# Optimization experiments

Measured on AMD Instinct MI355X. Metric: run time of the kernel, lower is better.

The kernel has to match this reference:

```python
import jax, jax.numpy as jnp
import numpy as np

N, D = 1024, 1024          # sensors, raw signal length
EMB, CC, TP, NH, L, FF = 128, 64, 16, 4, 2, 2048
HD = EMB // NH             # head dim = 32


def setup_inputs() -> dict:
    key = jax.random.key(0)
    ks = iter(jax.random.split(key, 64))
    rn = lambda shape, s=0.05: jax.random.normal(next(ks), shape, dtype=jnp.float32) * s
    return {
        "x": jax.random.normal(next(ks), (N, 1, D), dtype=jnp.float32),
        "conv1_w": rn((CC // 2, 1, 7), 0.3), "conv1_b": rn((CC // 2,)),
        "bn1_g": jnp.ones((CC // 2,)), "bn1_b": jnp.zeros((CC // 2,)),
        "bn1_m": jnp.zeros((CC // 2,)), "bn1_v": jnp.ones((CC // 2,)),
        "conv2_w": rn((CC, CC // 2, 5), 0.1), "conv2_b": rn((CC,)),
        "bn2_g": jnp.ones((CC,)), "bn2_b": jnp.zeros((CC,)),
        "bn2_m": jnp.zeros((CC,)), "bn2_v": jnp.ones((CC,)),
        "proj_w": rn((EMB, CC * TP)), "proj_b": rn((EMB,)),
        "attn_in_w": rn((L, 3 * EMB, EMB)), "attn_in_b": rn((L, 3 * EMB)),
        "attn_out_w": rn((L, EMB, EMB)), "attn_out_b": rn((L, EMB)),
        "ln1_g": jnp.ones((L, EMB)), "ln1_b": jnp.zeros((L, EMB)),
        "ff1_w": rn((L, FF, EMB)), "ff1_b": rn((L, FF)),
        "ff2_w": rn((L, EMB, FF)), "ff2_b": rn((L, EMB)),
        "ln2_g": jnp.ones((L, EMB)), "ln2_b": jnp.zeros((L, EMB)),
        "nh1_w": rn((EMB, EMB)), "nh1_b": rn((EMB,)),
        "nh2_w": rn((3, EMB)), "nh2_b": rn((3,)),
        "e1_w": rn((EMB, 2 * EMB)), "e1_b": rn((EMB,)),
        "e2_w": rn((1, EMB)), "e2_b": rn((1,)),
        "p1_w": rn((EMB, EMB)), "p1_b": rn((EMB,)),
        "p2_w": rn((EMB, EMB)), "p2_b": rn((EMB,)),
    }


def _conv1d(x, w, b, pad):
    y = jax.lax.conv_general_dilated(x, w, (1,), [(pad, pad)],
                                     dimension_numbers=("NCH", "OIH", "NCH"))
    return y + b[None, :, None]


def _bn(x, g, b, m, v):  # eval-mode BatchNorm1d, eps=1e-5
    return (x - m[None, :, None]) * (g / jnp.sqrt(v + 1e-5))[None, :, None] + b[None, :, None]


def _ln(x, g, b):  # LayerNorm over last dim, eps=1e-5
    mu = x.mean(-1, keepdims=True)
    var = ((x - mu) ** 2).mean(-1, keepdims=True)
    return (x - mu) / jnp.sqrt(var + 1e-5) * g + b


def reference(x, conv1_w, conv1_b, bn1_g, bn1_b, bn1_m, bn1_v,
              conv2_w, conv2_b, bn2_g, bn2_b, bn2_m, bn2_v,
              proj_w, proj_b, attn_in_w, attn_in_b, attn_out_w, attn_out_b,
              ln1_g, ln1_b, ff1_w, ff1_b, ff2_w, ff2_b, ln2_g, ln2_b,
              nh1_w, nh1_b, nh2_w, nh2_b, e1_w, e1_b, e2_w, e2_b,
              p1_w, p1_b, p2_w, p2_b):
    # ---- SensorTemporalEncoder: conv+BN+GELU x2, AdaptiveAvgPool1d(TP) ----
    h = jax.nn.gelu(_bn(_conv1d(x, conv1_w, conv1_b, 3), bn1_g, bn1_b, bn1_m, bn1_v), approximate=False)
    h = jax.nn.gelu(_bn(_conv1d(h, conv2_w, conv2_b, 2), bn2_g, bn2_b, bn2_m, bn2_v), approximate=False)
    h = h.reshape(N, CC, TP, D // TP).mean(-1)  # adaptive avg pool (D divisible by TP)
    z = h.reshape(N, CC * TP) @ proj_w.T + proj_b  # (N, EMB)

    # ---- TransformerEncoder (post-LN, relu FFN, eval: no dropout) ----
    t = z
    for l in range(L):
        qkv = t @ attn_in_w[l].T + attn_in_b[l]          # (N, 3*EMB)
        q, k, v = jnp.split(qkv, 3, axis=-1)
        q = q.reshape(N, NH, HD).transpose(1, 0, 2)      # (H, N, d)
        k = k.reshape(N, NH, HD).transpose(1, 0, 2)
        v = v.reshape(N, NH, HD).transpose(1, 0, 2)
        a = jax.nn.softmax(jnp.einsum("hnd,hmd->hnm", q, k) / (HD ** 0.5), axis=-1)
        o = jnp.einsum("hnm,hmd->hnd", a, v).transpose(1, 0, 2).reshape(N, EMB)
        t = _ln(t + o @ attn_out_w[l].T + attn_out_b[l], ln1_g[l], ln1_b[l])
        f = jax.nn.relu(t @ ff1_w[l].T + ff1_b[l]) @ ff2_w[l].T + ff2_b[l]
        t = _ln(t + f, ln2_g[l], ln2_b[l])

    # ---- node head ----
    node_logits = jax.nn.relu(t @ nh1_w.T + nh1_b) @ nh2_w.T + nh2_b  # (N, 3)

    # ---- all-pairs edge MLP: cat([hi,hj]) @ W1 == hi@W1[:,:E] + hj@W1[:,E:] ----
    hi = t @ e1_w[:, :EMB].T                 # (N, EMB)
    hj = t @ e1_w[:, EMB:].T                 # (N, EMB)
    pre = hi[:, None, :] + hj[None, :, :] + e1_b  # (N, N, EMB)
    edge_logits = (jax.nn.relu(pre) @ e2_w[0]) + e2_b[0]  # (N, N)

    # ---- projector on pre-transformer z ----
    proj = jax.nn.relu(z @ p1_w.T + p1_b) @ p2_w.T + p2_b  # (N, EMB)
    return (node_logits, edge_logits, proj)
```

## Files before the change

kernel.cpp:

```cpp
#include <hip/hip_runtime.h>
#include <math.h>


typedef float f32x4 __attribute__((ext_vector_type(4)));
typedef short bf16x8 __attribute__((ext_vector_type(8)));
typedef unsigned short u16;
typedef unsigned short us4 __attribute__((ext_vector_type(4)));
typedef unsigned int u32;

__device__ __forceinline__ float gelu_fast(float v) {
  float ax = fabsf(v) * 0.70710678118654752440f;
  float t = __builtin_amdgcn_rcpf(fmaf(0.3275911f, ax, 1.f));
  float p = fmaf(1.061405429f, t, -1.453152027f);
  p = fmaf(p, t, 1.421413741f);
  p = fmaf(p, t, -0.284496736f);
  p = fmaf(p, t, 0.254829592f);
  p = p * t;
  float e = __expf(-ax * ax);
  float erfa = fmaf(-p, e, 1.f);
  float erfv = copysignf(erfa, v);
  return 0.5f * v * (1.f + erfv);
}

__device__ __forceinline__ u16 to_bf16(float v) {
  u32 u = __float_as_uint(v);
  return (u16)((u + 0x7FFFu + ((u >> 16) & 1u)) >> 16);
}
__device__ __forceinline__ u32 packbf(float a, float b) {
  return (u32)to_bf16(a) | ((u32)to_bf16(b) << 16);
}

__global__ __launch_bounds__(256) void encoder_kernel(
    const float* __restrict__ x,
    const float* __restrict__ w1, const float* __restrict__ b1,
    const float* __restrict__ g1, const float* __restrict__ be1,
    const float* __restrict__ m1, const float* __restrict__ v1,
    const float* __restrict__ w2, const float* __restrict__ b2,
    const float* __restrict__ g2, const float* __restrict__ be2,
    const float* __restrict__ m2, const float* __restrict__ v2,
    u16* __restrict__ pooled_bf)
{
  const int blk = blockIdx.x;
  const int n = blk >> 1, hb = blk & 1;
  const int P0 = hb * 512;
  const int tid = threadIdx.x;

  __shared__ __align__(16) float xs[524];
  __shared__ __align__(16) u16 h1s[516 * 40];

  for (int s = tid; s < 522; s += 256) {
    int gp = P0 - 5 + s;
    xs[s] = (gp >= 0 && gp < 1024) ? x[n * 1024 + gp] : 0.f;
  }

  const int l = tid & 63;
  const int w = tid >> 6;
  const int col = l & 15;
  const int kh = l >> 4;
  const int oc = w * 16 + col;
  bf16x8 bf[5];
#pragma unroll
  for (int t = 0; t < 5; t++) {
#pragma unroll
    for (int e = 0; e < 8; e++)
      bf[t][e] = (short)to_bf16(w2[(oc * 32 + kh * 8 + e) * 5 + t]);
  }
  const float sc2 = g2[oc] * rsqrtf(v2[oc] + 1e-5f);
  const float sh2 = (b2[oc] - m2[oc]) * sc2 + be2[oc];

  const int ch = tid & 31;
  float wk[7];
#pragma unroll
  for (int k = 0; k < 7; k++) wk[k] = w1[ch * 7 + k];
  const float s1 = g1[ch] * rsqrtf(v1[ch] + 1e-5f);
  const float t1 = (b1[ch] - m1[ch]) * s1 + be1[ch];

  __syncthreads();

  const int rb = tid >> 5;
  for (int r = rb; r < 516; r += 8) {
    float acc = 0.f;
#pragma unroll
    for (int k = 0; k < 7; k++) acc += wk[k] * xs[r + k];
    int pos = P0 - 2 + r;
    u16 hv = to_bf16(gelu_fast(fmaf(acc, s1, t1)));
    h1s[r * 40 + ch] = (pos >= 0 && pos < 1024) ? hv : (u16)0;
  }
  __syncthreads();

  float pool = 0.f;
#pragma unroll 4
  for (int pt = 0; pt < 32; pt++) {
    f32x4 acc = {0.f, 0.f, 0.f, 0.f};
    const u16* ap = &h1s[(pt * 16 + col) * 40 + kh * 8];
#pragma unroll
    for (int t = 0; t < 5; t++) {
      bf16x8 af = *(const bf16x8*)(ap + t * 40);
      acc = __builtin_amdgcn_mfma_f32_16x16x32_bf16(af, bf[t], acc, 0, 0, 0);
    }
    float s = 0.f;
#pragma unroll
    for (int rr = 0; rr < 4; rr++) s += gelu_fast(fmaf(acc[rr], sc2, sh2));
    pool += s;
    if ((pt & 3) == 3) {
      pool += __shfl_xor(pool, 16);
      pool += __shfl_xor(pool, 32);
      if (l < 16)
        pooled_bf[(n * 64 + oc) * 16 + hb * 8 + (pt >> 2)] =
            to_bf16(pool * (1.f / 64.f));
      pool = 0.f;
    }
  }
}

__global__ __launch_bounds__(256) void wconv_kernel(
    const float* __restrict__ proj_w, const float* __restrict__ attn_in_w,
    const float* __restrict__ attn_out_w, const float* __restrict__ ff1_w,
    const float* __restrict__ ff2_w, const float* __restrict__ nh1_w,
    const float* __restrict__ e1_w, const float* __restrict__ e1_b,
    const float* __restrict__ p1_w, const float* __restrict__ p2_w,
    u16* __restrict__ wbf, float* __restrict__ wbias)
{
  if (blockIdx.x == 1360) {
    int j = threadIdx.x;
    wbias[j] = (j < 128) ? 0.f : e1_b[j - 128];
    return;
  }
  int i0 = (blockIdx.x * 256 + threadIdx.x) * 4;
  float v[4];
  if (i0 < 131072) {
    const float* s = proj_w + i0;
#pragma unroll
    for (int u = 0; u < 4; u++) v[u] = s[u];
  } else if (i0 < 229376) {
    const float* s = attn_in_w + (i0 - 131072);
#pragma unroll
    for (int u = 0; u < 4; u++) v[u] = s[u];
  } else if (i0 < 262144) {
    const float* s = attn_out_w + (i0 - 229376);
#pragma unroll
    for (int u = 0; u < 4; u++) v[u] = s[u];
  } else if (i0 < 786432) {
    const float* s = ff1_w + (i0 - 262144);
#pragma unroll
    for (int u = 0; u < 4; u++) v[u] = s[u];
  } else if (i0 < 1310720) {
    const float* s = ff2_w + (i0 - 786432);
#pragma unroll
    for (int u = 0; u < 4; u++) v[u] = s[u];
  } else if (i0 < 1327104) {
    const float* s = nh1_w + (i0 - 1310720);
#pragma unroll
    for (int u = 0; u < 4; u++) v[u] = s[u];
  } else if (i0 < 1359872) {
    int j = i0 - 1327104;
#pragma unroll
    for (int u = 0; u < 4; u++) {
      int idx = j + u, nn = idx >> 7, k = idx & 127;
      v[u] = e1_w[(nn & 127) * 256 + (nn >> 7) * 128 + k];
    }
  } else if (i0 < 1376256) {
    const float* s = p1_w + (i0 - 1359872);
#pragma unroll
    for (int u = 0; u < 4; u++) v[u] = s[u];
  } else {
    const float* s = p2_w + (i0 - 1376256);
#pragma unroll
    for (int u = 0; u < 4; u++) v[u] = s[u];
  }
  us4 o;
#pragma unroll
  for (int u = 0; u < 4; u++) o[u] = to_bf16(v[u]);
  *(us4*)(wbf + i0) = o;
}

template<int NR, bool RELU, bool VT>
__global__ __launch_bounds__(64) void mm_kernel(
    const u16* __restrict__ A, int lda,
    const u16* __restrict__ B, int ldb,
    const float* __restrict__ bias,
    float* __restrict__ Cf, u16* __restrict__ Cb, u16* __restrict__ vt,
    int ldc, int K)
{
  const int m0 = blockIdx.x * 32, n0 = blockIdx.y * (NR * 16);
  const int l = threadIdx.x;
  const int r = l & 15, kh = l >> 4;

  f32x4 acc[2][NR];
#pragma unroll
  for (int i = 0; i < 2; i++)
#pragma unroll
    for (int j = 0; j < NR; j++) acc[i][j] = (f32x4){0.f, 0.f, 0.f, 0.f};

  const u16* Ap0 = A + (size_t)(m0 + r) * lda + kh * 8;
  const u16* Ap1 = Ap0 + (size_t)16 * lda;
  const u16* Bp = B + (size_t)(n0 + r) * ldb + kh * 8;

  for (int k0 = 0; k0 < K; k0 += 32) {
    bf16x8 a0 = *(const bf16x8*)(Ap0 + k0);
    bf16x8 a1 = *(const bf16x8*)(Ap1 + k0);
    bf16x8 bfr[NR];
#pragma unroll
    for (int ni = 0; ni < NR; ni++)
      bfr[ni] = *(const bf16x8*)(Bp + (size_t)ni * 16 * ldb + k0);
#pragma unroll
    for (int ni = 0; ni < NR; ni++) {
      acc[0][ni] = __builtin_amdgcn_mfma_f32_16x16x32_bf16(a0, bfr[ni], acc[0][ni], 0, 0, 0);
      acc[1][ni] = __builtin_amdgcn_mfma_f32_16x16x32_bf16(a1, bfr[ni], acc[1][ni], 0, 0, 0);
    }
  }

#pragma unroll
  for (int mi = 0; mi < 2; mi++) {
#pragma unroll
    for (int ni = 0; ni < NR; ni++) {
#pragma unroll
      for (int reg = 0; reg < 4; reg++) {
        int row = m0 + mi * 16 + kh * 4 + reg;
        int colx = n0 + ni * 16 + r;
        float v = acc[mi][ni][reg];
        if (bias) v += bias[colx];
        if (RELU) v = fmaxf(v, 0.f);
        if (Cf) Cf[(size_t)row * ldc + colx] = v;
        if (Cb) Cb[(size_t)row * ldc + colx] = to_bf16(v);
        if (VT) {
          if (colx >= 256) {
            int hv = (colx - 256) >> 5, dv = (colx - 256) & 31;
            vt[(size_t)hv * 32768 + (size_t)dv * 1024 + row] = to_bf16(v);
          }
        }
      }
    }
  }
}

__global__ __launch_bounds__(64) void attn_kernel(
    const u16* __restrict__ qkv, const u16* __restrict__ vt,
    u16* __restrict__ attnO)
{
  const int h = blockIdx.y, q0 = blockIdx.x * 16;
  const int l = threadIdx.x, q = l & 15, g = l >> 4;
  const float iso = 0.17677669529663689f;

  bf16x8 qf = *(const bf16x8*)(qkv + (size_t)(q0 + q) * 384 + h * 32 + g * 8);
  const int kvo0 = 8 * (q >> 2) + (q & 3);
  const int kvo1 = kvo0 + 4;
  const u16* kbase = qkv + 128 + h * 32 + g * 8;
  const u16* vbase = vt + (size_t)h * 32768 + (size_t)q * 1024 + g * 8;

  f32x4 o0 = {0.f, 0.f, 0.f, 0.f}, o1 = {0.f, 0.f, 0.f, 0.f};
  float m = -1e30f, lsum = 0.f;
  const f32x4 zero = {0.f, 0.f, 0.f, 0.f};

  for (int kv0 = 0; kv0 < 1024; kv0 += 32) {
    bf16x8 k0f = *(const bf16x8*)(kbase + (size_t)(kv0 + kvo0) * 384);
    bf16x8 k1f = *(const bf16x8*)(kbase + (size_t)(kv0 + kvo1) * 384);
    f32x4 s0 = __builtin_amdgcn_mfma_f32_16x16x32_bf16(k0f, qf, zero, 0, 0, 0);
    f32x4 s1 = __builtin_amdgcn_mfma_f32_16x16x32_bf16(k1f, qf, zero, 0, 0, 0);

    float tm = fmaxf(fmaxf(fmaxf(s0[0], s0[1]), fmaxf(s0[2], s0[3])),
                     fmaxf(fmaxf(s1[0], s1[1]), fmaxf(s1[2], s1[3])));
    tm = fmaxf(tm, __shfl_xor(tm, 16));
    tm = fmaxf(tm, __shfl_xor(tm, 32));
    float mn = fmaxf(m, tm);
    float corr = __expf((m - mn) * iso);

    float e0[4], e1v[4], sum = 0.f;
#pragma unroll
    for (int j = 0; j < 4; j++) {
      e0[j] = __expf((s0[j] - mn) * iso);
      e1v[j] = __expf((s1[j] - mn) * iso);
      sum += e0[j] + e1v[j];
    }
    lsum = lsum * corr + sum;
#pragma unroll
    for (int j = 0; j < 4; j++) { o0[j] *= corr; o1[j] *= corr; }

    union { u32 u[4]; bf16x8 v; } P;
    P.u[0] = packbf(e0[0], e0[1]);
    P.u[1] = packbf(e0[2], e0[3]);
    P.u[2] = packbf(e1v[0], e1v[1]);
    P.u[3] = packbf(e1v[2], e1v[3]);

    bf16x8 v0 = *(const bf16x8*)(vbase + kv0);
    bf16x8 v1 = *(const bf16x8*)(vbase + 16 * 1024 + kv0);
    o0 = __builtin_amdgcn_mfma_f32_16x16x32_bf16(v0, P.v, o0, 0, 0, 0);
    o1 = __builtin_amdgcn_mfma_f32_16x16x32_bf16(v1, P.v, o1, 0, 0, 0);
    m = mn;
  }
  lsum += __shfl_xor(lsum, 16);
  lsum += __shfl_xor(lsum, 32);
  float inv = __builtin_amdgcn_rcpf(lsum);

  us4 w0, w1;
#pragma unroll
  for (int reg = 0; reg < 4; reg++) {
    w0[reg] = to_bf16(o0[reg] * inv);
    w1[reg] = to_bf16(o1[reg] * inv);
  }
  u16* outp = attnO + (size_t)(q0 + q) * 128 + h * 32 + 4 * g;
  *(us4*)outp = w0;
  *(us4*)(outp + 16) = w1;
}

template<int K>
__global__ __launch_bounds__(256) void owl_kernel(
    const u16* __restrict__ A, const u16* __restrict__ Bw,
    const float* __restrict__ bias, const float* __restrict__ Res,
    float* __restrict__ outF, u16* __restrict__ outB,
    const float* __restrict__ g_, const float* __restrict__ b_)
{
  __shared__ float ld[32][132];
  const int m0 = blockIdx.x * 32;
  const int tid = threadIdx.x;
  const int w = tid >> 6, l = tid & 63;
  const int r = l & 15, kg = l >> 4;

  f32x4 acc[2][2];
#pragma unroll
  for (int i = 0; i < 2; i++)
#pragma unroll
    for (int j = 0; j < 2; j++) acc[i][j] = (f32x4){0.f, 0.f, 0.f, 0.f};

  const u16* Ap0 = A + (size_t)(m0 + r) * K + kg * 8;
  const u16* Ap1 = Ap0 + (size_t)16 * K;
  const u16* Bp0 = Bw + (size_t)(w * 32 + r) * K + kg * 8;
  const u16* Bp1 = Bp0 + (size_t)16 * K;

#pragma unroll 4
  for (int k0 = 0; k0 < K; k0 += 32) {
    bf16x8 a0 = *(const bf16x8*)(Ap0 + k0);
    bf16x8 a1 = *(const bf16x8*)(Ap1 + k0);
    bf16x8 b0 = *(const bf16x8*)(Bp0 + k0);
    bf16x8 b1 = *(const bf16x8*)(Bp1 + k0);
    acc[0][0] = __builtin_amdgcn_mfma_f32_16x16x32_bf16(a0, b0, acc[0][0], 0, 0, 0);
    acc[0][1] = __builtin_amdgcn_mfma_f32_16x16x32_bf16(a0, b1, acc[0][1], 0, 0, 0);
    acc[1][0] = __builtin_amdgcn_mfma_f32_16x16x32_bf16(a1, b0, acc[1][0], 0, 0, 0);
    acc[1][1] = __builtin_amdgcn_mfma_f32_16x16x32_bf16(a1, b1, acc[1][1], 0, 0, 0);
  }

#pragma unroll
  for (int mi = 0; mi < 2; mi++)
#pragma unroll
    for (int ni = 0; ni < 2; ni++)
#pragma unroll
      for (int reg = 0; reg < 4; reg++) {
        int row = mi * 16 + kg * 4 + reg;
        int col = w * 32 + ni * 16 + r;
        ld[row][col] = acc[mi][ni][reg] + bias[col] +
                       Res[(size_t)(m0 + row) * 128 + col];
      }
  __syncthreads();

  const int row = tid >> 3, s8 = tid & 7;
  f32x4 vv[4];
  float sum = 0.f, ss = 0.f;
#pragma unroll
  for (int u = 0; u < 4; u++) {
    vv[u] = *(const f32x4*)&ld[row][s8 * 16 + u * 4];
#pragma unroll
    for (int j = 0; j < 4; j++) { sum += vv[u][j]; ss += vv[u][j] * vv[u][j]; }
  }
#pragma unroll
  for (int off = 1; off <= 4; off <<= 1) {
    sum += __shfl_xor(sum, off);
    ss += __shfl_xor(ss, off);
  }
  float mu = sum * (1.f / 128.f);
  float var = ss * (1.f / 128.f) - mu * mu;
  float inv = rsqrtf(var + 1e-5f);
  size_t base = (size_t)(m0 + row) * 128;
#pragma unroll
  for (int u = 0; u < 4; u++) {
    int c = s8 * 16 + u * 4;
    f32x4 gv = *(const f32x4*)(g_ + c);
    f32x4 bv = *(const f32x4*)(b_ + c);
    f32x4 o;
    us4 ob;
#pragma unroll
    for (int j = 0; j < 4; j++) {
      o[j] = (vv[u][j] - mu) * inv * gv[j] + bv[j];
      ob[j] = to_bf16(o[j]);
    }
    *(f32x4*)(outF + base + c) = o;
    *(us4*)(outB + base + c) = ob;
  }
}

__global__ __launch_bounds__(256) void nh2_kernel(
    const float* __restrict__ mid, const float* __restrict__ w,
    const float* __restrict__ b, float* __restrict__ out)
{
  int m = blockIdx.x * 256 + threadIdx.x;
  const float* row = mid + (size_t)m * 128;
  float a0 = 0.f, a1 = 0.f, a2 = 0.f;
#pragma unroll 4
  for (int k = 0; k < 128; k++) {
    float xv = row[k];
    a0 += xv * w[k]; a1 += xv * w[128 + k]; a2 += xv * w[256 + k];
  }
  out[m * 3 + 0] = a0 + b[0];
  out[m * 3 + 1] = a1 + b[1];
  out[m * 3 + 2] = a2 + b[2];
}

__global__ __launch_bounds__(256) void edge_kernel(
    const float* __restrict__ comb,
    const float* __restrict__ w, const float* __restrict__ e2b,
    float* __restrict__ out)
{
  const int i0 = blockIdx.x * 64;
  const int j0 = blockIdx.y * 32;
  __shared__ float his[128][64];
  __shared__ float hjs[128][32];
  const int tid = threadIdx.x;
  {
    int r = tid >> 2, c0 = (tid & 3) * 32;
#pragma unroll
    for (int u = 0; u < 8; u++) {
      float4 v = *(const float4*)(comb + (size_t)(i0 + r) * 256 + c0 + u * 4);
      his[c0 + u * 4 + 0][r] = v.x; his[c0 + u * 4 + 1][r] = v.y;
      his[c0 + u * 4 + 2][r] = v.z; his[c0 + u * 4 + 3][r] = v.w;
    }
  }
  {
    int r = tid >> 3, c0 = (tid & 7) * 16;
#pragma unroll
    for (int u = 0; u < 4; u++) {
      float4 v = *(const float4*)(comb + (size_t)(j0 + r) * 256 + 128 + c0 + u * 4);
      hjs[c0 + u * 4 + 0][r] = v.x; hjs[c0 + u * 4 + 1][r] = v.y;
      hjs[c0 + u * 4 + 2][r] = v.z; hjs[c0 + u * 4 + 3][r] = v.w;
    }
  }
  __syncthreads();
  const int il = (tid & 15) * 4, jl = (tid >> 4) * 2;
  float acc[4][2] = {{0.f,0.f},{0.f,0.f},{0.f,0.f},{0.f,0.f}};
  for (int e = 0; e < 128; e++) {
    float4 a = *(const float4*)&his[e][il];
    float2 bv = *(const float2*)&hjs[e][jl];
    float we = w[e];
    float av[4] = {a.x, a.y, a.z, a.w};
    float bb[2] = {bv.x, bv.y};
#pragma unroll
    for (int ii = 0; ii < 4; ii++)
#pragma unroll
      for (int jj = 0; jj < 2; jj++)
        acc[ii][jj] += fmaxf(av[ii] + bb[jj], 0.f) * we;
  }
  float eb = e2b[0];
#pragma unroll
  for (int ii = 0; ii < 4; ii++) {
    float2 vv = make_float2(acc[ii][0] + eb, acc[ii][1] + eb);
    *(float2*)(out + (size_t)(i0 + il + ii) * 1024 + j0 + jl) = vv;
  }
}

extern "C" void kernel_launch(void* const* d_in, const int* in_sizes, int n_in,
                              void* d_out, int out_size, void* d_ws, size_t ws_size,
                              hipStream_t stream)
{
  const float* x        = (const float*)d_in[0];
  const float* conv1_w  = (const float*)d_in[1];
  const float* conv1_b  = (const float*)d_in[2];
  const float* bn1_g    = (const float*)d_in[3];
  const float* bn1_b    = (const float*)d_in[4];
  const float* bn1_m    = (const float*)d_in[5];
  const float* bn1_v    = (const float*)d_in[6];
  const float* conv2_w  = (const float*)d_in[7];
  const float* conv2_b  = (const float*)d_in[8];
  const float* bn2_g    = (const float*)d_in[9];
  const float* bn2_b    = (const float*)d_in[10];
  const float* bn2_m    = (const float*)d_in[11];
  const float* bn2_v    = (const float*)d_in[12];
  const float* proj_w   = (const float*)d_in[13];
  const float* proj_b   = (const float*)d_in[14];
  const float* attn_in_w  = (const float*)d_in[15];
  const float* attn_in_b  = (const float*)d_in[16];
  const float* attn_out_w = (const float*)d_in[17];
  const float* attn_out_b = (const float*)d_in[18];
  const float* ln1_g    = (const float*)d_in[19];
  const float* ln1_b    = (const float*)d_in[20];
  const float* ff1_w    = (const float*)d_in[21];
  const float* ff1_b    = (const float*)d_in[22];
  const float* ff2_w    = (const float*)d_in[23];
  const float* ff2_b    = (const float*)d_in[24];
  const float* ln2_g    = (const float*)d_in[25];
  const float* ln2_b    = (const float*)d_in[26];
  const float* nh1_w    = (const float*)d_in[27];
  const float* nh1_b    = (const float*)d_in[28];
  const float* nh2_w    = (const float*)d_in[29];
  const float* nh2_b    = (const float*)d_in[30];
  const float* e1_w     = (const float*)d_in[31];
  const float* e1_b     = (const float*)d_in[32];
  const float* e2_w     = (const float*)d_in[33];
  const float* e2_b     = (const float*)d_in[34];
  const float* p1_w     = (const float*)d_in[35];
  const float* p1_b     = (const float*)d_in[36];
  const float* p2_w     = (const float*)d_in[37];
  const float* p2_b     = (const float*)d_in[38];

  float* ws = (float*)d_ws;

  u16*  wbf    = (u16*)ws;
  float* wbias = ws + 696320;
  float* z     = ws + 696576;
  u16*  z_bf   = (u16*)(ws + 827648);
  float* tS    = ws + 893184;
  u16*  t_bf   = (u16*)(ws + 1024256);
  u16*  qkv_bf = (u16*)(ws + 1089792);
  float* R     = ws + 1286400;
  u16*  pooled_bf = (u16*)R;
  u16*  attnO  = (u16*)R;
  u16*  vt     = (u16*)R + 131072;
  u16*  fb     = (u16*)R;
  float* nhmid = R;
  float* e1out = R + 131072;
  u16*  pmid   = (u16*)(R + 393216);

  float* out_node = (float*)d_out;
  float* out_edge = out_node + 3072;
  float* out_proj = out_edge + 1048576;

  float* nullf = nullptr; u16* nullb = nullptr;

  wconv_kernel<<<1361, 256, 0, stream>>>(
      proj_w, attn_in_w, attn_out_w, ff1_w, ff2_w, nh1_w, e1_w, e1_b,
      p1_w, p2_w, wbf, wbias);

  encoder_kernel<<<2048, 256, 0, stream>>>(
      x, conv1_w, conv1_b, bn1_g, bn1_b, bn1_m, bn1_v,
      conv2_w, conv2_b, bn2_g, bn2_b, bn2_m, bn2_v, pooled_bf);

  mm_kernel<2, false, false><<<dim3(32, 4), 64, 0, stream>>>(
      pooled_bf, 1024, wbf, 1024, proj_b, z, z_bf, nullb, 128, 1024);

  for (int l = 0; l < 2; l++) {
    const float* resIn = l ? tS : z;
    const u16* tin_bf = l ? t_bf : z_bf;
    mm_kernel<4, false, true><<<dim3(32, 6), 64, 0, stream>>>(
        tin_bf, 128, wbf + 131072 + l * 49152, 128, attn_in_b + l * 384,
        nullf, qkv_bf, vt, 384, 128);
    attn_kernel<<<dim3(64, 4), 64, 0, stream>>>(qkv_bf, vt, attnO);
    owl_kernel<128><<<32, 256, 0, stream>>>(
        attnO, wbf + 229376 + l * 16384, attn_out_b + l * 128, resIn,
        tS, t_bf, ln1_g + l * 128, ln1_b + l * 128);
    mm_kernel<4, true, false><<<dim3(32, 32), 64, 0, stream>>>(
        t_bf, 128, wbf + 262144 + l * 262144, 128, ff1_b + l * 2048,
        nullf, fb, nullb, 2048, 128);
    owl_kernel<2048><<<32, 256, 0, stream>>>(
        fb, wbf + 786432 + l * 262144, ff2_b + l * 128, tS,
        tS, t_bf, ln2_g + l * 128, ln2_b + l * 128);
  }

  mm_kernel<2, true, false><<<dim3(32, 4), 64, 0, stream>>>(
      t_bf, 128, wbf + 1310720, 128, nh1_b, nhmid, nullb, nullb, 128, 128);
  nh2_kernel<<<4, 256, 0, stream>>>(nhmid, nh2_w, nh2_b, out_node);

  mm_kernel<2, false, false><<<dim3(32, 8), 64, 0, stream>>>(
      t_bf, 128, wbf + 1327104, 128, wbias, e1out, nullb, nullb, 256, 128);
  edge_kernel<<<dim3(16, 32), 256, 0, stream>>>(e1out, e2_w, e2_b, out_edge);

  mm_kernel<2, true, false><<<dim3(32, 4), 64, 0, stream>>>(
      z_bf, 128, wbf + 1359872, 128, p1_b, nullf, pmid, nullb, 128, 128);
  mm_kernel<2, false, false><<<dim3(32, 4), 64, 0, stream>>>(
      pmid, 128, wbf + 1376256, 128, p2_b, out_proj, nullb, nullb, 128, 128);
}
```

Baseline: 447.6 us.

## Split FF2+LayerNorm into wider GEMM plus row-norm, prefetch attention K/V, compile-time K

The fused FF2 GEMM with LayerNorm ran on only 32 blocks. It is replaced by an mm_kernel launch over 64 blocks that writes pre-activations, followed by a separate warp-per-row residual LayerNorm kernel. The attention loop now double-buffers its K and V fragments by loading the next tile before computing on the current one. mm_kernel takes K as a template parameter with unroll 4, and nh2 spreads each row across four lanes with the weights staged in shared memory. The trade is an extra launch and an extra round trip of the FF2 output through global memory, in exchange for more parallelism and better load latency hiding.

```diff
diff --git a/kernel.cpp b/kernel.cpp
--- a/kernel.cpp
+++ b/kernel.cpp
@@ -174,13 +174,13 @@
   *(us4*)(wbf + i0) = o;
 }
 
-template<int NR, bool RELU, bool VT>
+template<int NR, int K, bool RELU, bool VT>
 __global__ __launch_bounds__(64) void mm_kernel(
     const u16* __restrict__ A, int lda,
     const u16* __restrict__ B, int ldb,
     const float* __restrict__ bias,
     float* __restrict__ Cf, u16* __restrict__ Cb, u16* __restrict__ vt,
-    int ldc, int K)
+    int ldc)
 {
   const int m0 = blockIdx.x * 32, n0 = blockIdx.y * (NR * 16);
   const int l = threadIdx.x;
@@ -196,6 +196,7 @@
   const u16* Ap1 = Ap0 + (size_t)16 * lda;
   const u16* Bp = B + (size_t)(n0 + r) * ldb + kh * 8;
 
+#pragma unroll 4
   for (int k0 = 0; k0 < K; k0 += 32) {
     bf16x8 a0 = *(const bf16x8*)(Ap0 + k0);
     bf16x8 a1 = *(const bf16x8*)(Ap1 + k0);
@@ -252,11 +253,20 @@
   float m = -1e30f, lsum = 0.f;
   const f32x4 zero = {0.f, 0.f, 0.f, 0.f};
 
+  bf16x8 k0c = *(const bf16x8*)(kbase + (size_t)kvo0 * 384);
+  bf16x8 k1c = *(const bf16x8*)(kbase + (size_t)kvo1 * 384);
+  bf16x8 v0c = *(const bf16x8*)(vbase);
+  bf16x8 v1c = *(const bf16x8*)(vbase + 16 * 1024);
+
   for (int kv0 = 0; kv0 < 1024; kv0 += 32) {
-    bf16x8 k0f = *(const bf16x8*)(kbase + (size_t)(kv0 + kvo0) * 384);
-    bf16x8 k1f = *(const bf16x8*)(kbase + (size_t)(kv0 + kvo1) * 384);
-    f32x4 s0 = __builtin_amdgcn_mfma_f32_16x16x32_bf16(k0f, qf, zero, 0, 0, 0);
-    f32x4 s1 = __builtin_amdgcn_mfma_f32_16x16x32_bf16(k1f, qf, zero, 0, 0, 0);
+    const int nx = (kv0 + 32 < 1024) ? kv0 + 32 : kv0;
+    bf16x8 k0n = *(const bf16x8*)(kbase + (size_t)(nx + kvo0) * 384);
+    bf16x8 k1n = *(const bf16x8*)(kbase + (size_t)(nx + kvo1) * 384);
+    bf16x8 v0n = *(const bf16x8*)(vbase + nx);
+    bf16x8 v1n = *(const bf16x8*)(vbase + 16 * 1024 + nx);
+
+    f32x4 s0 = __builtin_amdgcn_mfma_f32_16x16x32_bf16(k0c, qf, zero, 0, 0, 0);
+    f32x4 s1 = __builtin_amdgcn_mfma_f32_16x16x32_bf16(k1c, qf, zero, 0, 0, 0);
 
     float tm = fmaxf(fmaxf(fmaxf(s0[0], s0[1]), fmaxf(s0[2], s0[3])),
                      fmaxf(fmaxf(s1[0], s1[1]), fmaxf(s1[2], s1[3])));
@@ -282,11 +292,10 @@
     P.u[2] = packbf(e1v[0], e1v[1]);
     P.u[3] = packbf(e1v[2], e1v[3]);
 
-    bf16x8 v0 = *(const bf16x8*)(vbase + kv0);
-    bf16x8 v1 = *(const bf16x8*)(vbase + 16 * 1024 + kv0);
-    o0 = __builtin_amdgcn_mfma_f32_16x16x32_bf16(v0, P.v, o0, 0, 0, 0);
-    o1 = __builtin_amdgcn_mfma_f32_16x16x32_bf16(v1, P.v, o1, 0, 0, 0);
+    o0 = __builtin_amdgcn_mfma_f32_16x16x32_bf16(v0c, P.v, o0, 0, 0, 0);
+    o1 = __builtin_amdgcn_mfma_f32_16x16x32_bf16(v1c, P.v, o1, 0, 0, 0);
     m = mn;
+    k0c = k0n; k1c = k1n; v0c = v0n; v1c = v1n;
   }
   lsum += __shfl_xor(lsum, 16);
   lsum += __shfl_xor(lsum, 32);
@@ -303,7 +312,6 @@
   *(us4*)(outp + 16) = w1;
 }
 
-template<int K>
 __global__ __launch_bounds__(256) void owl_kernel(
     const u16* __restrict__ A, const u16* __restrict__ Bw,
     const float* __restrict__ bias, const float* __restrict__ Res,
@@ -322,13 +330,13 @@
 #pragma unroll
     for (int j = 0; j < 2; j++) acc[i][j] = (f32x4){0.f, 0.f, 0.f, 0.f};
 
-  const u16* Ap0 = A + (size_t)(m0 + r) * K + kg * 8;
-  const u16* Ap1 = Ap0 + (size_t)16 * K;
-  const u16* Bp0 = Bw + (size_t)(w * 32 + r) * K + kg * 8;
-  const u16* Bp1 = Bp0 + (size_t)16 * K;
-
-#pragma unroll 4
-  for (int k0 = 0; k0 < K; k0 += 32) {
+  const u16* Ap0 = A + (size_t)(m0 + r) * 128 + kg * 8;
+  const u16* Ap1 = Ap0 + (size_t)16 * 128;
+  const u16* Bp0 = Bw + (size_t)(w * 32 + r) * 128 + kg * 8;
+  const u16* Bp1 = Bp0 + (size_t)16 * 128;
+
+#pragma unroll
+  for (int k0 = 0; k0 < 128; k0 += 32) {
     bf16x8 a0 = *(const bf16x8*)(Ap0 + k0);
     bf16x8 a1 = *(const bf16x8*)(Ap1 + k0);
     bf16x8 b0 = *(const bf16x8*)(Bp0 + k0);
@@ -387,21 +395,63 @@
   }
 }
 
+__global__ __launch_bounds__(256) void ln2r_kernel(
+    const float* __restrict__ pre, float* __restrict__ tS, u16* __restrict__ t_bf,
+    const float* __restrict__ g_, const float* __restrict__ b_)
+{
+  int row = blockIdx.x * 4 + (threadIdx.x >> 6);
+  int lane = threadIdx.x & 63;
+  size_t idx = (size_t)row * 128 + lane * 2;
+  float2 pv = *(const float2*)(pre + idx);
+  float2 rv = *(const float2*)(tS + idx);
+  float vx = pv.x + rv.x, vy = pv.y + rv.y;
+  float s = vx + vy;
+#pragma unroll
+  for (int off = 32; off >= 1; off >>= 1) s += __shfl_xor(s, off);
+  float mu = s * (1.f / 128.f);
+  float dx = vx - mu, dy = vy - mu;
+  float q = dx * dx + dy * dy;
+#pragma unroll
+  for (int off = 32; off >= 1; off >>= 1) q += __shfl_xor(q, off);
+  float inv = rsqrtf(q * (1.f / 128.f) + 1e-5f);
+  float2 gv = *(const float2*)(g_ + lane * 2);
+  float2 bv = *(const float2*)(b_ + lane * 2);
+  float ox = dx * inv * gv.x + bv.x, oy = dy * inv * gv.y + bv.y;
+  tS[idx] = ox; tS[idx + 1] = oy;
+  t_bf[idx] = to_bf16(ox); t_bf[idx + 1] = to_bf16(oy);
+}
+
 __global__ __launch_bounds__(256) void nh2_kernel(
     const float* __restrict__ mid, const float* __restrict__ w,
     const float* __restrict__ b, float* __restrict__ out)
 {
-  int m = blockIdx.x * 256 + threadIdx.x;
-  const float* row = mid + (size_t)m * 128;
+  __shared__ float wsm[384];
+  for (int i = threadIdx.x; i < 384; i += 256) wsm[i] = w[i];
+  __syncthreads();
+  int r = blockIdx.x * 64 + (threadIdx.x >> 2);
+  int q = threadIdx.x & 3;
+  const float* rp = mid + (size_t)r * 128 + q * 32;
   float a0 = 0.f, a1 = 0.f, a2 = 0.f;
-#pragma unroll 4
-  for (int k = 0; k < 128; k++) {
-    float xv = row[k];
-    a0 += xv * w[k]; a1 += xv * w[128 + k]; a2 += xv * w[256 + k];
-  }
-  out[m * 3 + 0] = a0 + b[0];
-  out[m * 3 + 1] = a1 + b[1];
-  out[m * 3 + 2] = a2 + b[2];
+#pragma unroll
+  for (int u = 0; u < 8; u++) {
+    float4 v = *(const float4*)(rp + u * 4);
+    int k = q * 32 + u * 4;
+    float xv[4] = {v.x, v.y, v.z, v.w};
+#pragma unroll
+    for (int j = 0; j < 4; j++) {
+      a0 += xv[j] * wsm[k + j];
+      a1 += xv[j] * wsm[128 + k + j];
+      a2 += xv[j] * wsm[256 + k + j];
+    }
+  }
+  a0 += __shfl_xor(a0, 1); a0 += __shfl_xor(a0, 2);
+  a1 += __shfl_xor(a1, 1); a1 += __shfl_xor(a1, 2);
+  a2 += __shfl_xor(a2, 1); a2 += __shfl_xor(a2, 2);
+  if (q == 0) {
+    out[r * 3 + 0] = a0 + b[0];
+    out[r * 3 + 1] = a1 + b[1];
+    out[r * 3 + 2] = a2 + b[2];
+  }
 }
 
 __global__ __launch_bounds__(256) void edge_kernel(
@@ -508,7 +558,8 @@
   float* tS    = ws + 893184;
   u16*  t_bf   = (u16*)(ws + 1024256);
   u16*  qkv_bf = (u16*)(ws + 1089792);
-  float* R     = ws + 1286400;
+  float* pre   = ws + 1286400;
+  float* R     = ws + 1417472;
   u16*  pooled_bf = (u16*)R;
   u16*  attnO  = (u16*)R;
   u16*  vt     = (u16*)R + 131072;
@@ -531,37 +582,39 @@
       x, conv1_w, conv1_b, bn1_g, bn1_b, bn1_m, bn1_v,
       conv2_w, conv2_b, bn2_g, bn2_b, bn2_m, bn2_v, pooled_bf);
 
-  mm_kernel<2, false, false><<<dim3(32, 4), 64, 0, stream>>>(
-      pooled_bf, 1024, wbf, 1024, proj_b, z, z_bf, nullb, 128, 1024);
+  mm_kernel<2, 1024, false, false><<<dim3(32, 4), 64, 0, stream>>>(
+      pooled_bf, 1024, wbf, 1024, proj_b, z, z_bf, nullb, 128);
 
   for (int l = 0; l < 2; l++) {
     const float* resIn = l ? tS : z;
     const u16* tin_bf = l ? t_bf : z_bf;
-    mm_kernel<4, false, true><<<dim3(32, 6), 64, 0, stream>>>(
+    mm_kernel<4, 128, false, true><<<dim3(32, 6), 64, 0, stream>>>(
         tin_bf, 128, wbf + 131072 + l * 49152, 128, attn_in_b + l * 384,
-        nullf, qkv_bf, vt, 384, 128);
+        nullf, qkv_bf, vt, 384);
     attn_kernel<<<dim3(64, 4), 64, 0, stream>>>(qkv_bf, vt, attnO);
-    owl_kernel<128><<<32, 256, 0, stream>>>(
+    owl_kernel<<<32, 256, 0, stream>>>(
         attnO, wbf + 229376 + l * 16384, attn_out_b + l * 128, resIn,
         tS, t_bf, ln1_g + l * 128, ln1_b + l * 128);
-    mm_kernel<4, true, false><<<dim3(32, 32), 64, 0, stream>>>(
+    mm_kernel<4, 128, true, false><<<dim3(32, 32), 64, 0, stream>>>(
         t_bf, 128, wbf + 262144 + l * 262144, 128, ff1_b + l * 2048,
-        nullf, fb, nullb, 2048, 128);
-    owl_kernel<2048><<<32, 256, 0, stream>>>(
-        fb, wbf + 786432 + l * 262144, ff2_b + l * 128, tS,
-        tS, t_bf, ln2_g + l * 128, ln2_b + l * 128);
-  }
-
-  mm_kernel<2, true, false><<<dim3(32, 4), 64, 0, stream>>>(
-      t_bf, 128, wbf + 1310720, 128, nh1_b, nhmid, nullb, nullb, 128, 128);
-  nh2_kernel<<<4, 256, 0, stream>>>(nhmid, nh2_w, nh2_b, out_node);
-
-  mm_kernel<2, false, false><<<dim3(32, 8), 64, 0, stream>>>(
-      t_bf, 128, wbf + 1327104, 128, wbias, e1out, nullb, nullb, 256, 128);
+        nullf, fb, nullb, 2048);
+    mm_kernel<4, 2048, false, false><<<dim3(32, 2), 64, 0, stream>>>(
+        fb, 2048, wbf + 786432 + l * 262144, 2048, ff2_b + l * 128,
+        pre, nullb, nullb, 128);
+    ln2r_kernel<<<256, 256, 0, stream>>>(
+        pre, tS, t_bf, ln2_g + l * 128, ln2_b + l * 128);
+  }
+
+  mm_kernel<2, 128, true, false><<<dim3(32, 4), 64, 0, stream>>>(
+      t_bf, 128, wbf + 1310720, 128, nh1_b, nhmid, nullb, nullb, 128);
+  nh2_kernel<<<16, 256, 0, stream>>>(nhmid, nh2_w, nh2_b, out_node);
+
+  mm_kernel<2, 128, false, false><<<dim3(32, 8), 64, 0, stream>>>(
+      t_bf, 128, wbf + 1327104, 128, wbias, e1out, nullb, nullb, 256);
   edge_kernel<<<dim3(16, 32), 256, 0, stream>>>(e1out, e2_w, e2_b, out_edge);
 
-  mm_kernel<2, true, false><<<dim3(32, 4), 64, 0, stream>>>(
-      z_bf, 128, wbf + 1359872, 128, p1_b, nullf, pmid, nullb, 128, 128);
-  mm_kernel<2, false, false><<<dim3(32, 4), 64, 0, stream>>>(
-      pmid, 128, wbf + 1376256, 128, p2_b, out_proj, nullb, nullb, 128, 128);
-}
+  mm_kernel<2, 128, true, false><<<dim3(32, 4), 64, 0, stream>>>(
+      z_bf, 128, wbf + 1359872, 128, p1_b, nullf, pmid, nullb, 128);
+  mm_kernel<2, 128, false, false><<<dim3(32, 4), 64, 0, stream>>>(
+      pmid, 128, wbf + 1376256, 128, p2_b, out_proj, nullb, nullb, 128);
+}
```

New measurement: 422.4 us. -5.6%, faster.
